# Optimization experiments

Measured on AMD Instinct MI355X. Metric: run time of the kernel, lower is better.

Reference implementation:

```python
import jax, jax.numpy as jnp
import numpy as np

D_MODEL = 768
D_AU = 5
D_VIS = 20
BOT = 64
WIN = 7
SCALE = 1.0 / np.sqrt(BOT).astype(np.float32)


def layernorm(x, w, b, eps=1e-5):
    mu = jnp.mean(x, axis=-1, keepdims=True)
    var = jnp.mean(jnp.square(x - mu), axis=-1, keepdims=True)
    return (x - mu) * jax.lax.rsqrt(var + eps) * w + b


def proximity_bias_matrix(prox_bias, L_a, L_v):
    # |i * (L_v/L_a) - j|, floored to int; gather into learned table, -inf outside window
    ai = jnp.arange(L_a, dtype=jnp.float32) * (L_v / L_a)  # [L_a]
    vj = jnp.arange(L_v, dtype=jnp.float32)                # [L_v]
    dist = jnp.floor(jnp.abs(ai[:, None] - vj[None, :])).astype(jnp.int32)  # [L_a, L_v]
    within = dist <= WIN
    gathered = prox_bias[jnp.clip(dist, 0, 2 * WIN)]
    return jnp.where(within, gathered, -jnp.inf)


def setup_inputs() -> dict:
    key = jax.random.key(0)
    ks = jax.random.split(key, 32)
    B, L_t, L_v, L_a = 32, 1024, 1024, 2048
    std = 0.02
    inp = {
        'x_text': jax.random.normal(ks[0], (B, L_t, D_MODEL), jnp.float32),
        'video_features': jax.random.normal(ks[1], (B, L_v, D_VIS), jnp.float32),
        'audio_features': jax.random.normal(ks[2], (B, L_a, D_AU), jnp.float32),
        # adapter input LayerNorm (BERT init: weight=1, bias=0)
        'ln_w': jnp.ones((D_MODEL,), jnp.float32),
        'ln_b': jnp.zeros((D_MODEL,), jnp.float32),
        # down projections (torch Linear: [out, in])
        'dpa_w': std * jax.random.normal(ks[3], (BOT, D_AU), jnp.float32),
        'dpa_b': jnp.zeros((BOT,), jnp.float32),
        'dpv_w': std * jax.random.normal(ks[4], (BOT, D_VIS), jnp.float32),
        'dpv_b': jnp.zeros((BOT,), jnp.float32),
        # audio->video cross attention
        'wq_a': std * jax.random.normal(ks[5], (BOT, BOT), jnp.float32),
        'wk_v': std * jax.random.normal(ks[6], (BOT, BOT), jnp.float32),
        'wv_v': std * jax.random.normal(ks[7], (BOT, BOT), jnp.float32),
        'prox_bias': jnp.zeros((2 * WIN + 1,), jnp.float32),
        # fusion MLP + LN
        'fln_w': jnp.ones((2 * BOT,), jnp.float32),
        'fln_b': jnp.zeros((2 * BOT,), jnp.float32),
        'w1f_w': std * jax.random.normal(ks[8], (BOT, 2 * BOT), jnp.float32),
        'w1f_b': jnp.zeros((BOT,), jnp.float32),
        'w2f_w': std * jax.random.normal(ks[9], (BOT, BOT), jnp.float32),
        'w2f_b': jnp.zeros((BOT,), jnp.float32),
        # text->sync alignment attention
        'wq_t': std * jax.random.normal(ks[10], (BOT, D_MODEL), jnp.float32),
        'wk_s': std * jax.random.normal(ks[11], (BOT, BOT), jnp.float32),
        'wv_s': std * jax.random.normal(ks[12], (BOT, BOT), jnp.float32),
        # up projection + learnable scalar
        'up_w': std * jax.random.normal(ks[13], (D_MODEL, BOT), jnp.float32),
        'up_b': jnp.zeros((D_MODEL,), jnp.float32),
        'scale': jnp.ones((1,), jnp.float32),
    }
    return inp


def reference(x_text, video_features, audio_features, ln_w, ln_b, dpa_w, dpa_b,
              dpv_w, dpv_b, wq_a, wk_v, wv_v, prox_bias, fln_w, fln_b,
              w1f_w, w1f_b, w2f_w, w2f_b, wq_t, wk_s, wv_s, up_w, up_b, scale):
    L_v = video_features.shape[1]
    L_a = audio_features.shape[1]
    # adapter_layernorm_option == 'in'
    xt = layernorm(x_text, ln_w, ln_b)
    # down projections + ReLU
    H_v = jax.nn.relu(jnp.einsum('bvf,df->bvd', video_features, dpv_w) + dpv_b)
    H_a = jax.nn.relu(jnp.einsum('baf,df->bad', audio_features, dpa_w) + dpa_b)
    # audio queries attend to video keys/values with proximity bias
    Q_a = jnp.einsum('bad,ed->bae', H_a, wq_a)
    K_v = jnp.einsum('bvd,ed->bve', H_v, wk_v)
    V_v = jnp.einsum('bvd,ed->bve', H_v, wv_v)
    scores = jnp.einsum('bad,bvd->bav', Q_a, K_v) * SCALE
    scores = scores + proximity_bias_matrix(prox_bias, L_a, L_v)[None]
    A = jax.nn.softmax(scores, axis=-1)  # dropout: eval-mode identity
    H_v_tilde = jnp.einsum('bav,bvd->bad', A, V_v)
    # fusion
    H_av = jnp.concatenate([H_a, H_v_tilde], axis=-1)  # [B, L_a, 2*BOT]
    H_av_n = layernorm(H_av, fln_w, fln_b)
    H_fused = jax.nn.relu(jnp.einsum('bac,dc->bad', H_av_n, w1f_w) + w1f_b)
    H_sync = jnp.einsum('bad,ed->bae', H_fused, w2f_w) + w2f_b
    # text -> sync alignment attention
    Q_t = jnp.einsum('btm,dm->btd', xt, wq_t)
    K_s = jnp.einsum('bad,ed->bae', H_sync, wk_s)
    V_s = jnp.einsum('bad,ed->bae', H_sync, wv_s)
    align = jax.nn.softmax(jnp.einsum('btd,bad->bta', Q_t, K_s) * SCALE, axis=-1)
    H_align = jnp.einsum('bta,bad->btd', align, V_s)
    up = jnp.einsum('btd,md->btm', H_align, up_w) + up_b
    return up * scale
```

## Files before the change

### kernel.cpp

```cpp
#include <hip/hip_runtime.h>

typedef unsigned short u16;
typedef unsigned int u32;

using frag8 = __attribute__((ext_vector_type(8))) short;
using facc4 = __attribute__((ext_vector_type(4))) float;

__device__ __forceinline__ float b2f(u16 u) {
  union { u32 i; float f; } v; v.i = ((u32)u) << 16; return v.f;
}
__device__ __forceinline__ u16 f2b(float f) {
  union { float f; u32 i; } v; v.f = f;
  u32 u = v.i;
  return (u16)((u + 0x7FFFu + ((u >> 16) & 1u)) >> 16);
}
__device__ __forceinline__ float ldin(const void* p, size_t i, bool bf) {
  return bf ? b2f(((const u16*)p)[i]) : ((const float*)p)[i];
}
__device__ __forceinline__ u16 ldb(const void* p, size_t i, bool bf) {
  return bf ? ((const u16*)p)[i] : f2b(((const float*)p)[i]);
}
__device__ __forceinline__ bool dt_bf16(const void* ones) {
  return *(const u32*)ones == 0x3F803F80u;
}
__device__ __forceinline__ void gload_lds16(const void* g, void* l) {
  __builtin_amdgcn_global_load_lds(
      (__attribute__((address_space(1))) void*)(g),
      (__attribute__((address_space(3))) void*)(l), 16, 0, 0);
}

#define LT 1024
#define LV 1024
#define LA 2048
#define DM 768

#define W_QA 0
#define W_KV 4096
#define W_VV 8192
#define W_1F 12288
#define W_2F 20480
#define W_KS 24576
#define W_VS 28672
#define W_UP 32768
#define W_QT 81920
#define W_TOT 131072

__global__ __launch_bounds__(256) void k_prep(
    const void* __restrict__ wqa, const void* __restrict__ wkv, const void* __restrict__ wvv,
    const void* __restrict__ w1f, const void* __restrict__ w2f,
    const void* __restrict__ wks, const void* __restrict__ wvs,
    const void* __restrict__ wup, const void* __restrict__ wqt, const void* __restrict__ lnw,
    u16* __restrict__ W)
{
  bool bf = dt_bf16(lnw);
  int idx = blockIdx.x * 256 + threadIdx.x;
  if (idx >= W_TOT) return;
  u16 v;
  if      (idx < W_KV) v = ldb(wqa, idx - W_QA, bf);
  else if (idx < W_VV) v = ldb(wkv, idx - W_KV, bf);
  else if (idx < W_1F) v = ldb(wvv, idx - W_VV, bf);
  else if (idx < W_2F) v = ldb(w1f, idx - W_1F, bf);
  else if (idx < W_KS) v = ldb(w2f, idx - W_2F, bf);
  else if (idx < W_VS) v = ldb(wks, idx - W_KS, bf);
  else if (idx < W_UP) v = ldb(wvs, idx - W_VS, bf);
  else if (idx < W_QT) v = ldb(wup, idx - W_UP, bf);
  else {
    int r = idx - W_QT;
    int k = r - (r / DM) * DM;
    v = f2b(ldin(wqt, r, bf) * ldin(lnw, k, bf));
  }
  W[idx] = v;
}

__global__ __launch_bounds__(256) void k_const(
    const u16* __restrict__ W, const void* __restrict__ wqt, const void* __restrict__ lnb,
    const void* __restrict__ dtp, float* __restrict__ CC)
{
  bool bf = dt_bf16(dtp);
  int j = blockIdx.x * 8 + (threadIdx.x >> 5);
  int lane32 = threadIdx.x & 31;
  float s = 0.f;
  if (j < 64) {
    for (int k = lane32; k < DM; k += 32) s += b2f(W[W_QT + (size_t)j * DM + k]);
  } else {
    int e = j - 64;
    for (int k = lane32; k < DM; k += 32)
      s += ldin(lnb, k, bf) * ldin(wqt, (size_t)e * DM + k, bf);
  }
#pragma unroll
  for (int m = 1; m < 32; m <<= 1) s += __shfl_xor(s, m);
  if (lane32 == 0) CC[j] = s;
}

__global__ __launch_bounds__(256) void k_video(
    const void* __restrict__ vid, const void* __restrict__ dpv_w, const void* __restrict__ dpv_b,
    const u16* __restrict__ W, const void* __restrict__ dtp,
    u16* __restrict__ KvG, u16* __restrict__ VvTG)
{
  bool bf = dt_bf16(dtp);
  __shared__ float vidT[20][72];
  __shared__ float dpvT[20][72];
  __shared__ float dpvB[64];
  __shared__ u16 hvL[64][72];
  __shared__ u16 ksS[64][72];
  __shared__ u16 vsS[64][72];
  int tid = threadIdx.x;
  int b = blockIdx.x >> 4, v0 = (blockIdx.x & 15) << 6;
  for (int c = tid; c < 1280; c += 256) {
    int row = c / 20, d = c - row * 20;
    vidT[d][row] = ldin(vid, (size_t)(b * LV + v0) * 20 + c, bf);
    dpvT[d][row] = ldin(dpv_w, c, bf);
  }
  if (tid < 64) dpvB[tid] = ldin(dpv_b, tid, bf);
  __syncthreads();
  int w = tid >> 6, ln = tid & 63;
  int quad = ln >> 4, l16 = ln & 15;
  for (int rr = 0; rr < 16; ++rr) {
    int row = w * 16 + rr;
    float h = dpvB[ln];
#pragma unroll
    for (int d = 0; d < 20; ++d) h += vidT[d][row] * dpvT[d][ln];
    hvL[row][ln] = f2b(fmaxf(h, 0.f));
  }
  facc4 ka[4] = {}, va[4] = {};
#pragma unroll
  for (int kk = 0; kk < 2; ++kk) {
    frag8 af = *(const frag8*)&hvL[w * 16 + l16][kk * 32 + quad * 8];
#pragma unroll
    for (int nt = 0; nt < 4; ++nt) {
      frag8 bk = *(const frag8*)(W + W_KV + (size_t)(nt * 16 + l16) * 64 + kk * 32 + quad * 8);
      frag8 bv = *(const frag8*)(W + W_VV + (size_t)(nt * 16 + l16) * 64 + kk * 32 + quad * 8);
      ka[nt] = __builtin_amdgcn_mfma_f32_16x16x32_bf16(af, bk, ka[nt], 0, 0, 0);
      va[nt] = __builtin_amdgcn_mfma_f32_16x16x32_bf16(af, bv, va[nt], 0, 0, 0);
    }
  }
#pragma unroll
  for (int nt = 0; nt < 4; ++nt)
#pragma unroll
    for (int r = 0; r < 4; ++r) {
      int row = w * 16 + quad * 4 + r;
      ksS[row][nt * 16 + l16] = f2b(ka[nt][r]);
      vsS[row][nt * 16 + l16] = f2b(va[nt][r]);
    }
  __syncthreads();
  for (int c = tid; c < 2048; c += 256) {
    int row = c >> 5, sg = c & 31;
    u32 v = (u32)ksS[row][sg * 2] | ((u32)ksS[row][sg * 2 + 1] << 16);
    *(u32*)(KvG + (size_t)(b * LV + v0 + row) * 64 + sg * 2) = v;
  }
  for (int c = tid; c < 2048; c += 256) {
    int e = c >> 5, sg = c & 31;
    u32 v = (u32)vsS[sg * 2][e] | ((u32)vsS[sg * 2 + 1][e] << 16);
    *(u32*)(VvTG + (size_t)(b * 64 + e) * LV + v0 + sg * 2) = v;
  }
}

__global__ __launch_bounds__(256, 4) void k_lnqt(
    const void* __restrict__ x, const u16* __restrict__ W, const float* __restrict__ CC,
    const void* __restrict__ dtp, u16* __restrict__ Qt)
{
  bool bf = dt_bf16(dtp);
  __shared__ __align__(16) char pool[40960];
  int tid = threadIdx.x;
  int w = tid >> 6, ln = tid & 63;
  int quad = ln >> 4, l16 = ln & 15;
  int rt = w >> 1;
  int nt0 = (w & 1) * 2;
  int R0 = blockIdx.x * 32;
  facc4 acc[2] = {};
  float s = 0.f, ss = 0.f;

  if (!bf) {
    int rq = ln >> 4;
    const char* xb = (const char*)x + (size_t)R0 * 3072;
    const char* p0 = xb + (size_t)(w * 8 + rq) * 3072 + (((ln & 15) ^ rq) << 4);
    const char* p1 = xb + (size_t)(w * 8 + 4 + rq) * 3072 + (((ln & 15) ^ (4 + rq)) << 4);
    const char* wgA = (const char*)(W + W_QT) +
        (size_t)(w * 16 + (ln >> 3)) * 1536 + (((ln & 7) ^ (ln >> 3)) << 4);
    const char* wgB = wgA + 8 * 1536;

#define STAGE_X(BUF, T) do { \
    size_t o_ = (size_t)(T) * 256; \
    char* lb_ = pool + (BUF) * 8192 + w * 2048; \
    gload_lds16(p0 + o_, lb_); \
    gload_lds16(p1 + o_, lb_ + 1024); \
  } while (0)

#define STAGE_W(BUF, T) do { \
    size_t o_ = (size_t)(T) * 128; \
    char* wb_ = pool + 24576 + (BUF) * 8192 + w * 2048; \
    gload_lds16(wgA + o_, wb_); \
    gload_lds16(wgB + o_, wb_ + 1024); \
  } while (0)

    int rbase = (rt * 16 + l16) * 256;
    int r8 = l16 & 7;
    int c0a = rbase + (((quad * 2) ^ r8) << 4);
    int c0b = rbase + (((quad * 2 + 1) ^ r8) << 4);
    int c1a = rbase + (((8 + quad * 2) ^ r8) << 4);
    int c1b = rbase + (((9 + quad * 2) ^ r8) << 4);
    int wo0 = l16 * 128 + ((quad ^ r8) << 4);
    int wo1 = l16 * 128 + (((4 + quad) ^ r8) << 4);

#define COMPUTE(XB, WB) do { \
    const char* xt_ = pool + (XB) * 8192; \
    const char* wt_ = pool + 24576 + (WB) * 8192; \
    _Pragma("unroll") \
    for (int ks = 0; ks < 2; ++ks) { \
      float4 v0 = *(const float4*)(xt_ + (ks ? c1a : c0a)); \
      float4 v1 = *(const float4*)(xt_ + (ks ? c1b : c0b)); \
      s += v0.x + v0.y + v0.z + v0.w + v1.x + v1.y + v1.z + v1.w; \
      ss += v0.x * v0.x + v0.y * v0.y + v0.z * v0.z + v0.w * v0.w \
          + v1.x * v1.x + v1.y * v1.y + v1.z * v1.z + v1.w * v1.w; \
      union { u16 a[8]; frag8 f; } af; \
      af.a[0] = f2b(v0.x); af.a[1] = f2b(v0.y); af.a[2] = f2b(v0.z); af.a[3] = f2b(v0.w); \
      af.a[4] = f2b(v1.x); af.a[5] = f2b(v1.y); af.a[6] = f2b(v1.z); af.a[7] = f2b(v1.w); \
      int wo_ = ks ? wo1 : wo0; \
      _Pragma("unroll") \
      for (int n = 0; n < 2; ++n) { \
        frag8 bfr = *(const frag8*)(wt_ + wo_ + (nt0 + n) * 2048); \
        acc[n] = __builtin_amdgcn_mfma_f32_16x16x32_bf16(af.f, bfr, acc[n], 0, 0, 0); \
      } \
    } \
  } while (0)

#define ITERA(T, XC, XN, WN) do { \
    asm volatile("s_waitcnt vmcnt(2)" ::: "memory"); \
    __builtin_amdgcn_s_barrier(); \
    STAGE_W(WN, (T) + 1); \
    STAGE_X(XN, (T) + 2); \
    COMPUTE(XC, (T) & 1); \
  } while (0)

    STAGE_W(0, 0);
    STAGE_X(0, 0);
    STAGE_X(1, 1);
    ITERA(0, 0, 2, 1);
    ITERA(1, 1, 0, 0);
    ITERA(2, 2, 1, 1);
    ITERA(3, 0, 2, 0);
    ITERA(4, 1, 0, 1);
    ITERA(5, 2, 1, 0);
    ITERA(6, 0, 2, 1);
    ITERA(7, 1, 0, 0);
    ITERA(8, 2, 1, 1);
    ITERA(9, 0, 2, 0);
    asm volatile("s_waitcnt vmcnt(2)" ::: "memory");
    __builtin_amdgcn_s_barrier();
    STAGE_W(1, 11);
    COMPUTE(1, 0);
    asm volatile("s_waitcnt vmcnt(0)" ::: "memory");
    __builtin_amdgcn_s_barrier();
    COMPUTE(2, 1);

#undef ITERA
#undef COMPUTE
#undef STAGE_W
#undef STAGE_X
  } else {
    const u16* xrowb = (const u16*)x + (size_t)(R0 + rt * 16 + l16) * DM + quad * 8;
    for (int c = 0; c < 24; ++c) {
      union { u16 a[8]; frag8 f; } af;
      af.f = *(const frag8*)(xrowb + c * 32);
#pragma unroll
      for (int jj = 0; jj < 8; ++jj) { float v = b2f(af.a[jj]); s += v; ss += v * v; }
      int col = c * 32 + quad * 8;
#pragma unroll
      for (int n = 0; n < 2; ++n) {
        frag8 bfr = *(const frag8*)(W + W_QT + (size_t)((nt0 + n) * 16 + l16) * DM + col);
        acc[n] = __builtin_amdgcn_mfma_f32_16x16x32_bf16(af.f, bfr, acc[n], 0, 0, 0);
      }
    }
  }

  s += __shfl_xor(s, 16); ss += __shfl_xor(ss, 16);
  s += __shfl_xor(s, 32); ss += __shfl_xor(ss, 32);
  float mu = s * (1.f / 768.f);
  float var = ss * (1.f / 768.f) - mu * mu;
  float rs = rsqrtf(var + 1e-5f);
  float muR[4], rsR[4];
#pragma unroll
  for (int r = 0; r < 4; ++r) {
    muR[r] = __shfl(mu, quad * 4 + r);
    rsR[r] = __shfl(rs, quad * 4 + r);
  }
#pragma unroll
  for (int n = 0; n < 2; ++n) {
    int ntg = nt0 + n;
    float c1 = CC[ntg * 16 + l16], c2 = CC[64 + ntg * 16 + l16];
#pragma unroll
    for (int r = 0; r < 4; ++r) {
      int lrow = rt * 16 + quad * 4 + r;
      Qt[(size_t)(R0 + lrow) * 64 + ntg * 16 + l16] =
          f2b((acc[n][r] - muR[r] * c1) * rsR[r] * 0.125f + c2 * 0.125f);
    }
  }
}

__global__ __launch_bounds__(256, 4) void k_audio(
    const void* __restrict__ audio, const void* __restrict__ dpa_w, const void* __restrict__ dpa_b,
    const void* __restrict__ prox_b,
    const void* __restrict__ fln_w, const void* __restrict__ fln_b,
    const void* __restrict__ w1f_b, const void* __restrict__ w2f_b,
    const u16* __restrict__ W, const void* __restrict__ dtp,
    const u16* __restrict__ KvG, const u16* __restrict__ VvTG,
    u16* __restrict__ KsG, u16* __restrict__ VsTG)
{
  bool bf = dt_bf16(dtp);
  __shared__ __align__(16) char pool[36928];
  u16* S0   = (u16*)pool;
  u16* qL   = (u16*)(pool + 9216);
  u16* hnL  = (u16*)(pool + 18432);
  u16* vsS  = (u16*)(pool + 9216);
  float* flnw = (float*)(pool + 35840);
  float* flnb = (float*)(pool + 36352);
  float* prox = (float*)(pool + 36864);

  int tid = threadIdx.x;
  int b = blockIdx.x >> 5, i0 = (blockIdx.x & 31) << 6;
  int w = tid >> 6, ln = tid & 63;
  int quad = ln >> 4, l16 = ln & 15;
  int jbase = (i0 >> 1) - 8;

  if (tid >= 64 && tid < 192) { int t = tid - 64; flnw[t] = ldin(fln_w, t, bf); flnb[t] = ldin(fln_b, t, bf); }
  if (tid >= 192 && tid < 207) prox[tid - 192] = ldin(prox_b, tid - 192, bf);
  __syncthreads();

  float haF[4][4];
  {
    frag8 au = {};
    if (quad == 0) {
      size_t base = (size_t)(b * LA + i0 + w * 16 + l16) * 5;
#pragma unroll
      for (int k = 0; k < 5; ++k) au[k] = (short)ldb(audio, base + k, bf);
    }
#pragma unroll
    for (int nt = 0; nt < 4; ++nt) {
      frag8 bd = {};
      if (quad == 0) {
#pragma unroll
        for (int k = 0; k < 5; ++k) bd[k] = (short)ldb(dpa_w, (size_t)(nt * 16 + l16) * 5 + k, bf);
      }
      facc4 z = {};
      facc4 ha = __builtin_amdgcn_mfma_f32_16x16x32_bf16(au, bd, z, 0, 0, 0);
      float dB = ldin(dpa_b, nt * 16 + l16, bf);
#pragma unroll
      for (int r = 0; r < 4; ++r) {
        u16 hb = f2b(fmaxf(ha[r] + dB, 0.f));
        S0[(w * 16 + quad * 4 + r) * 72 + nt * 16 + l16] = hb;
        haF[nt][r] = b2f(hb);
      }
    }
  }
  {
    facc4 qa[4] = {};
#pragma unroll
    for (int kk = 0; kk < 2; ++kk) {
      frag8 af = *(const frag8*)&S0[(w * 16 + l16) * 72 + kk * 32 + quad * 8];
#pragma unroll
      for (int nt = 0; nt < 4; ++nt) {
        frag8 bfr = *(const frag8*)(W + W_QA + (size_t)(nt * 16 + l16) * 64 + kk * 32 + quad * 8);
        qa[nt] = __builtin_amdgcn_mfma_f32_16x16x32_bf16(af, bfr, qa[nt], 0, 0, 0);
      }
    }
#pragma unroll
    for (int nt = 0; nt < 4; ++nt)
#pragma unroll
      for (int r = 0; r < 4; ++r)
        qL[(w * 16 + quad * 4 + r) * 72 + nt * 16 + l16] = f2b(qa[nt][r] * 0.125f);
  }
  float inv[4];
  {
    facc4 sa[3] = {};
#pragma unroll
    for (int kk = 0; kk < 2; ++kk) {
      frag8 af = *(const frag8*)&qL[(w * 16 + l16) * 72 + kk * 32 + quad * 8];
#pragma unroll
      for (int nt = 0; nt < 3; ++nt) {
        int jj = jbase + nt * 16 + l16;
        jj = jj < 0 ? 0 : (jj > LV - 1 ? LV - 1 : jj);
        frag8 bfr = *(const frag8*)(KvG + ((size_t)(b * LV + jj) << 6) + kk * 32 + quad * 8);
        sa[nt] = __builtin_amdgcn_mfma_f32_16x16x32_bf16(af, bfr, sa[nt], 0, 0, 0);
      }
    }
    float den[4] = {0.f, 0.f, 0.f, 0.f};
#pragma unroll
    for (int nt = 0; nt < 3; ++nt)
#pragma unroll
      for (int r = 0; r < 4; ++r) {
        int row16 = quad * 4 + r;
        int i = i0 + w * 16 + row16;
        int j = jbase + nt * 16 + l16;
        float dist = fabsf((float)i * 0.5f - (float)j);
        float p = 0.f;
        if (j >= 0 && j < LV && dist < 8.f)
          p = exp2f(fminf(sa[nt][r] + prox[(int)dist], 60.f) * 1.44269504f);
        u16 pb = f2b(p);
        den[r] += b2f(pb);
        S0[(w * 16 + row16) * 72 + nt * 16 + l16] = pb;
      }
#pragma unroll
    for (int r = 0; r < 4; ++r) {
      S0[(w * 16 + quad * 4 + r) * 72 + 48 + l16] = 0;
#pragma unroll
      for (int m = 1; m < 16; m <<= 1) den[r] += __shfl_xor(den[r], m);
      inv[r] = 1.f / den[r];
    }
  }
  float hvF[4][4];
  {
    facc4 ha[4] = {};
#pragma unroll
    for (int kk = 0; kk < 2; ++kk) {
      frag8 af = *(const frag8*)&S0[(w * 16 + l16) * 72 + kk * 32 + quad * 8];
#pragma unroll
      for (int nt = 0; nt < 4; ++nt) {
        const u16* vp = VvTG + (size_t)(b * 64 + nt * 16 + l16) * LV;
        frag8 bfr = *(const frag8*)(vp + jbase + kk * 32 + quad * 8);
        ha[nt] = __builtin_amdgcn_mfma_f32_16x16x32_bf16(af, bfr, ha[nt], 0, 0, 0);
      }
    }
#pragma unroll
    for (int nt = 0; nt < 4; ++nt)
#pragma unroll
      for (int r = 0; r < 4; ++r) {
        u16 hb = f2b(ha[nt][r] * inv[r]);
        hvF[nt][r] = b2f(hb);
      }
  }
  __syncthreads();
#pragma unroll
  for (int r = 0; r < 4; ++r) {
    float s = 0.f, ss = 0.f;
#pragma unroll
    for (int nt = 0; nt < 4; ++nt) {
      float a = haF[nt][r], c = hvF[nt][r];
      s += a + c; ss += a * a + c * c;
    }
#pragma unroll
    for (int m = 1; m < 16; m <<= 1) { s += __shfl_xor(s, m); ss += __shfl_xor(ss, m); }
    float mu = s * (1.f / 128.f);
    float var = ss * (1.f / 128.f) - mu * mu;
    float rs = rsqrtf(var + 1e-5f);
    int row = w * 16 + quad * 4 + r;
#pragma unroll
    for (int nt = 0; nt < 4; ++nt) {
      int col = nt * 16 + l16;
      hnL[row * 136 + col]      = f2b((haF[nt][r] - mu) * rs * flnw[col] + flnb[col]);
      hnL[row * 136 + 64 + col] = f2b((hvF[nt][r] - mu) * rs * flnw[64 + col] + flnb[64 + col]);
    }
  }
  {
    facc4 f1[4] = {};
#pragma unroll
    for (int kk = 0; kk < 4; ++kk) {
      frag8 af = *(const frag8*)&hnL[(w * 16 + l16) * 136 + kk * 32 + quad * 8];
#pragma unroll
      for (int nt = 0; nt < 4; ++nt) {
        frag8 bfr = *(const frag8*)(W + W_1F + (size_t)(nt * 16 + l16) * 128 + kk * 32 + quad * 8);
        f1[nt] = __builtin_amdgcn_mfma_f32_16x16x32_bf16(af, bfr, f1[nt], 0, 0, 0);
      }
    }
#pragma unroll
    for (int nt = 0; nt < 4; ++nt) {
      float b1 = ldin(w1f_b, nt * 16 + l16, bf);
#pragma unroll
      for (int r = 0; r < 4; ++r)
        S0[(w * 16 + quad * 4 + r) * 72 + nt * 16 + l16] = f2b(fmaxf(f1[nt][r] + b1, 0.f));
    }
  }
  {
    facc4 f2[4] = {};
#pragma unroll
    for (int kk = 0; kk < 2; ++kk) {
      frag8 af = *(const frag8*)&S0[(w * 16 + l16) * 72 + kk * 32 + quad * 8];
#pragma unroll
      for (int nt = 0; nt < 4; ++nt) {
        frag8 bfr = *(const frag8*)(W + W_2F + (size_t)(nt * 16 + l16) * 64 + kk * 32 + quad * 8);
        f2[nt] = __builtin_amdgcn_mfma_f32_16x16x32_bf16(af, bfr, f2[nt], 0, 0, 0);
      }
    }
#pragma unroll
    for (int nt = 0; nt < 4; ++nt) {
      float b2 = ldin(w2f_b, nt * 16 + l16, bf);
#pragma unroll
      for (int r = 0; r < 4; ++r)
        S0[(w * 16 + quad * 4 + r) * 72 + nt * 16 + l16] = f2b(f2[nt][r] + b2);
    }
  }
  {
    facc4 fk[4] = {}, fv[4] = {};
#pragma unroll
    for (int kk = 0; kk < 2; ++kk) {
      frag8 af = *(const frag8*)&S0[(w * 16 + l16) * 72 + kk * 32 + quad * 8];
#pragma unroll
      for (int nt = 0; nt < 4; ++nt) {
        frag8 bk = *(const frag8*)(W + W_KS + (size_t)(nt * 16 + l16) * 64 + kk * 32 + quad * 8);
        frag8 bv = *(const frag8*)(W + W_VS + (size_t)(nt * 16 + l16) * 64 + kk * 32 + quad * 8);
        fk[nt] = __builtin_amdgcn_mfma_f32_16x16x32_bf16(af, bk, fk[nt], 0, 0, 0);
        fv[nt] = __builtin_amdgcn_mfma_f32_16x16x32_bf16(af, bv, fv[nt], 0, 0, 0);
      }
    }
#pragma unroll
    for (int nt = 0; nt < 4; ++nt)
#pragma unroll
      for (int r = 0; r < 4; ++r) {
        int row = w * 16 + quad * 4 + r;
        S0[row * 72 + nt * 16 + l16]  = f2b(fk[nt][r]);
        vsS[row * 72 + nt * 16 + l16] = f2b(fv[nt][r]);
      }
  }
  __syncthreads();
  for (int c = tid; c < 2048; c += 256) {
    int row = c >> 5, sg = c & 31;
    u32 v = (u32)S0[row * 72 + sg * 2] | ((u32)S0[row * 72 + sg * 2 + 1] << 16);
    *(u32*)(KsG + (size_t)(b * LA + i0 + row) * 64 + sg * 2) = v;
  }
  for (int c = tid; c < 2048; c += 256) {
    int e = c >> 5, sg = c & 31;
    u32 v = (u32)vsS[sg * 2 * 72 + e] | ((u32)vsS[(sg * 2 + 1) * 72 + e] << 16);
    *(u32*)(VsTG + (size_t)(b * 64 + e) * LA + i0 + sg * 2) = v;
  }
}

#define KS_OFF 0
#define VT_OFF 16384
#define PO_OFF 32768

__global__ __launch_bounds__(256, 4) void k_attn_p(
    const u16* __restrict__ Qt, const u16* __restrict__ KsG, const u16* __restrict__ VsT,
    u16* __restrict__ OpG, float* __restrict__ DenG)
{
  __shared__ __align__(16) char pool[40960];
  int tid = threadIdx.x, w = tid >> 6, ln = tid & 63;
  int quad = ln >> 4, l16 = ln & 15;
  int pb = blockIdx.x;
  int b = pb >> 5, tt = (pb >> 1) & 15, half = pb & 1;
  int t0 = tt << 6;
  const u16* qp = Qt + (size_t)(b * LT + t0 + w * 16 + l16) * 64;
  frag8 qf0 = *(const frag8*)(qp + quad * 8);
  frag8 qf1 = *(const frag8*)(qp + 32 + quad * 8);

  int r8 = ln >> 3;
  int sgx = (ln & 7) ^ r8;
  const char* kg0 = (const char*)KsG +
      (((size_t)(b * LA + half * 1024 + w * 16 + r8)) << 7) + sgx * 16;
  const char* kg1 = kg0 + 1024;
  const char* vg0 = (const char*)VsT +
      (((size_t)(b * 64 + w * 16 + r8)) * LA + half * 1024 + sgx * 8) * 2;
  const char* vg1 = vg0 + (size_t)8 * LA * 2;

#define STAGE(BUF, TT) do { \
    size_t ko_ = (size_t)(TT) * 8192, vo_ = (size_t)(TT) * 128; \
    gload_lds16(kg0 + ko_, pool + KS_OFF + (BUF) * 8192 + w * 2048); \
    gload_lds16(kg1 + ko_, pool + KS_OFF + (BUF) * 8192 + w * 2048 + 1024); \
    gload_lds16(vg0 + vo_, pool + VT_OFF + (BUF) * 8192 + w * 2048); \
    gload_lds16(vg1 + vo_, pool + VT_OFF + (BUF) * 8192 + w * 2048 + 1024); \
  } while (0)

  int l8 = l16 & 7, lh = l16 >> 3;
  int swl = l8 << 4;
  int koff0 = l16 * 128 + ((quad * 16) ^ swl);
  int koff1 = l16 * 128 + ((64 + quad * 16) ^ swl);
  int pro0 = w * 2048 + l16 * 128 + ((quad ^ l8) << 4);
  int pro1 = w * 2048 + l16 * 128 + (((4 + quad) ^ l8) << 4);
  int pwb = w * 2048 + quad * 512 + l8 * 2;

  facc4 oacc[4] = {};
  float den[4] = {0.f, 0.f, 0.f, 0.f};

#define COMPUTE(CUR) do { \
    const char* ksp_ = pool + KS_OFF + (CUR) * 8192; \
    const char* vtp_ = pool + VT_OFF + (CUR) * 8192; \
    __builtin_amdgcn_s_setprio(1); \
    _Pragma("unroll") \
    for (int nt = 0; nt < 4; ++nt) { \
      frag8 b0 = *(const frag8*)(ksp_ + koff0 + nt * 2048); \
      frag8 b1 = *(const frag8*)(ksp_ + koff1 + nt * 2048); \
      facc4 sv = {}; \
      sv = __builtin_amdgcn_mfma_f32_16x16x32_bf16(qf0, b0, sv, 0, 0, 0); \
      sv = __builtin_amdgcn_mfma_f32_16x16x32_bf16(qf1, b1, sv, 0, 0, 0); \
      _Pragma("unroll") \
      for (int r = 0; r < 4; ++r) { \
        float p = exp2f(fminf(sv[r], 60.f) * 1.44269504f); \
        u16 pb_ = f2b(p); \
        den[r] += b2f(pb_); \
        int rm_ = ((quad & 1) << 2) + r; \
        *(u16*)(pool + PO_OFF + pwb + r * 128 + (((nt * 2 + lh) ^ rm_) << 4)) = pb_; \
      } \
    } \
    _Pragma("unroll") \
    for (int kk = 0; kk < 2; ++kk) { \
      frag8 af = *(const frag8*)(pool + PO_OFF + (kk ? pro1 : pro0)); \
      _Pragma("unroll") \
      for (int nt = 0; nt < 4; ++nt) { \
        frag8 bv = *(const frag8*)(vtp_ + (kk ? koff1 : koff0) + nt * 2048); \
        oacc[nt] = __builtin_amdgcn_mfma_f32_16x16x32_bf16(af, bv, oacc[nt], 0, 0, 0); \
      } \
    } \
    __builtin_amdgcn_s_setprio(0); \
  } while (0)

#define ITERS(TT, CUR) do { \
    asm volatile("s_waitcnt vmcnt(0)" ::: "memory"); \
    __builtin_amdgcn_s_barrier(); \
    STAGE((CUR) ^ 1, (TT) + 1); \
    COMPUTE(CUR); \
  } while (0)

  STAGE(0, 0);
  for (int t2 = 0; t2 < 14; t2 += 2) {
    ITERS(t2, 0);
    ITERS(t2 + 1, 1);
  }
  ITERS(14, 0);
  asm volatile("s_waitcnt vmcnt(0)" ::: "memory");
  __builtin_amdgcn_s_barrier();
  COMPUTE(1);

#undef ITERS
#undef COMPUTE
#undef STAGE

#pragma unroll
  for (int m = 1; m < 16; m <<= 1)
#pragma unroll
    for (int r = 0; r < 4; ++r) den[r] += __shfl_xor(den[r], m);
  if (l16 == 0) {
#pragma unroll
    for (int r = 0; r < 4; ++r)
      DenG[(size_t)pb * 64 + w * 16 + quad * 4 + r] = den[r];
  }
#pragma unroll
  for (int nt = 0; nt < 4; ++nt)
#pragma unroll
    for (int r = 0; r < 4; ++r)
      OpG[(size_t)pb * 4096 + (w * 16 + quad * 4 + r) * 64 + nt * 16 + l16] =
          f2b(oacc[nt][r]);
}

__global__ __launch_bounds__(256) void k_up(
    const u16* __restrict__ OpG, const float* __restrict__ DenG,
    const u16* __restrict__ W, const void* __restrict__ up_b,
    const void* __restrict__ scaleP, const void* __restrict__ dtp, void* __restrict__ outp)
{
  bool bf = dt_bf16(dtp);
  int tid = threadIdx.x, w = tid >> 6, ln = tid & 63;
  int quad = ln >> 4, l16 = ln & 15;
  int g = blockIdx.x;
  int b = g >> 5, tt = (g >> 1) & 15, nh = g & 1;
  int t0 = tt << 6;
  int blk = b * 16 + tt;
  int row = w * 16 + l16;
  const u16* p0 = OpG + ((size_t)blk * 2 + 0) * 4096 + row * 64;
  const u16* p1 = p0 + 4096;
  float dsum = DenG[(size_t)blk * 128 + row] + DenG[(size_t)blk * 128 + 64 + row];
  float inv = 1.f / dsum;
  union { u16 a[8]; frag8 f; } a0, a1;
  {
    frag8 u0 = *(const frag8*)(p0 + quad * 8);
    frag8 u1 = *(const frag8*)(p1 + quad * 8);
    frag8 v0 = *(const frag8*)(p0 + 32 + quad * 8);
    frag8 v1 = *(const frag8*)(p1 + 32 + quad * 8);
#pragma unroll
    for (int j = 0; j < 8; ++j) {
      a0.a[j] = f2b((b2f((u16)u0[j]) + b2f((u16)u1[j])) * inv);
      a1.a[j] = f2b((b2f((u16)v0[j]) + b2f((u16)v1[j])) * inv);
    }
  }
  float scl = ldin(scaleP, 0, bf);
  u16* o16 = (u16*)outp;
  float* o32 = (float*)outp;
  for (int nt = nh * 24; nt < nh * 24 + 24; ++nt) {
    frag8 b0f = *(const frag8*)(W + W_UP + (size_t)(nt * 16 + l16) * 64 + quad * 8);
    frag8 b1f = *(const frag8*)(W + W_UP + (size_t)(nt * 16 + l16) * 64 + 32 + quad * 8);
    facc4 d = {};
    d = __builtin_amdgcn_mfma_f32_16x16x32_bf16(a0.f, b0f, d, 0, 0, 0);
    d = __builtin_amdgcn_mfma_f32_16x16x32_bf16(a1.f, b1f, d, 0, 0, 0);
    float ub = ldin(up_b, nt * 16 + l16, bf);
#pragma unroll
    for (int r = 0; r < 4; ++r) {
      int t = t0 + w * 16 + quad * 4 + r;
      size_t idx = ((size_t)(b * LT) + t) * DM + nt * 16 + l16;
      float v = (d[r] + ub) * scl;
      if (bf) o16[idx] = f2b(v); else o32[idx] = v;
    }
  }
}

extern "C" void kernel_launch(void* const* d_in, const int* in_sizes, int n_in,
                              void* d_out, int out_size, void* d_ws, size_t ws_size,
                              hipStream_t stream) {
  const void* x_text = d_in[0];
  const void* video  = d_in[1];
  const void* audio  = d_in[2];
  const void* ln_w   = d_in[3];
  const void* ln_b   = d_in[4];
  const void* dpa_w  = d_in[5];
  const void* dpa_b  = d_in[6];
  const void* dpv_w  = d_in[7];
  const void* dpv_b  = d_in[8];
  const void* wq_a   = d_in[9];
  const void* wk_v   = d_in[10];
  const void* wv_v   = d_in[11];
  const void* prox   = d_in[12];
  const void* fln_w  = d_in[13];
  const void* fln_b  = d_in[14];
  const void* w1f_w  = d_in[15];
  const void* w1f_b  = d_in[16];
  const void* w2f_w  = d_in[17];
  const void* w2f_b  = d_in[18];
  const void* wq_t   = d_in[19];
  const void* wk_s   = d_in[20];
  const void* wv_s   = d_in[21];
  const void* up_w   = d_in[22];
  const void* up_b   = d_in[23];
  const void* scale  = d_in[24];

  char* ws = (char*)d_ws;
  u16* KvG  = (u16*)(ws);
  u16* VvTG = (u16*)(ws + 4194304);
  u16* Qt   = (u16*)(ws + 8388608);
  u16* KsG  = (u16*)(ws + 12582912);
  u16* VsTG = (u16*)(ws + 20971520);
  u16* W    = (u16*)(ws + 29360128);
  float* CC = (float*)(ws + 29622272);
  u16* OpG  = (u16*)(ws);
  float* DenG = (float*)(ws + 29622784);

  k_prep <<<dim3(512), dim3(256), 0, stream>>>(wq_a, wk_v, wv_v, w1f_w, w2f_w,
                                               wk_s, wv_s, up_w, wq_t, ln_w, W);
  k_const<<<dim3(16),  dim3(256), 0, stream>>>(W, wq_t, ln_b, ln_w, CC);
  k_video<<<dim3(512), dim3(256), 0, stream>>>(video, dpv_w, dpv_b, W, ln_w, KvG, VvTG);
  k_lnqt <<<dim3(1024), dim3(256), 0, stream>>>(x_text, W, CC, ln_w, Qt);
  k_audio<<<dim3(1024), dim3(256), 0, stream>>>(audio, dpa_w, dpa_b, prox,
                                                fln_w, fln_b, w1f_b, w2f_b,
                                                W, ln_w, KvG, VvTG, KsG, VsTG);
  k_attn_p<<<dim3(1024), dim3(256), 0, stream>>>(Qt, KsG, VsTG, OpG, DenG);
  k_up   <<<dim3(1024), dim3(256), 0, stream>>>(OpG, DenG, W, up_b, scale, ln_w, d_out);
}
```

Measured before the change: 364.9 us.

## Merge independent prep, const, video, lnqt and audio kernels into two launches

Folds weight prep, the LN constant computation and the video projection into one launch by splitting on block index, and merges the text LN+Q projection with the audio branch into a second launch. This removes launch gaps and lets independent stages share the GPU concurrently. To break dependencies inside a launch, the constant and video parts now read raw weights directly instead of the prepped bf16 buffer, adding some redundant conversion work and scalar loads. The merged k_mid block carries the larger LDS pool of the two paths, which may lower occupancy for the audio blocks.

After: 394.8 us. 1.08x slower.

```diff
diff --git a/kernel.cpp b/kernel.cpp
--- a/kernel.cpp
+++ b/kernel.cpp
@@ -45,67 +45,67 @@
 #define W_QT 81920
 #define W_TOT 131072
 
-__global__ __launch_bounds__(256) void k_prep(
+__global__ __launch_bounds__(256) void k_stage0(
     const void* __restrict__ wqa, const void* __restrict__ wkv, const void* __restrict__ wvv,
     const void* __restrict__ w1f, const void* __restrict__ w2f,
     const void* __restrict__ wks, const void* __restrict__ wvs,
-    const void* __restrict__ wup, const void* __restrict__ wqt, const void* __restrict__ lnw,
-    u16* __restrict__ W)
+    const void* __restrict__ wup, const void* __restrict__ wqt,
+    const void* __restrict__ lnw, const void* __restrict__ lnb,
+    const void* __restrict__ vid, const void* __restrict__ dpv_w, const void* __restrict__ dpv_b,
+    u16* __restrict__ W, float* __restrict__ CC,
+    u16* __restrict__ KvG, u16* __restrict__ VvTG)
 {
   bool bf = dt_bf16(lnw);
-  int idx = blockIdx.x * 256 + threadIdx.x;
-  if (idx >= W_TOT) return;
-  u16 v;
-  if      (idx < W_KV) v = ldb(wqa, idx - W_QA, bf);
-  else if (idx < W_VV) v = ldb(wkv, idx - W_KV, bf);
-  else if (idx < W_1F) v = ldb(wvv, idx - W_VV, bf);
-  else if (idx < W_2F) v = ldb(w1f, idx - W_1F, bf);
-  else if (idx < W_KS) v = ldb(w2f, idx - W_2F, bf);
-  else if (idx < W_VS) v = ldb(wks, idx - W_KS, bf);
-  else if (idx < W_UP) v = ldb(wvs, idx - W_VS, bf);
-  else if (idx < W_QT) v = ldb(wup, idx - W_UP, bf);
-  else {
-    int r = idx - W_QT;
-    int k = r - (r / DM) * DM;
-    v = f2b(ldin(wqt, r, bf) * ldin(lnw, k, bf));
-  }
-  W[idx] = v;
-}
-
-__global__ __launch_bounds__(256) void k_const(
-    const u16* __restrict__ W, const void* __restrict__ wqt, const void* __restrict__ lnb,
-    const void* __restrict__ dtp, float* __restrict__ CC)
-{
-  bool bf = dt_bf16(dtp);
-  int j = blockIdx.x * 8 + (threadIdx.x >> 5);
-  int lane32 = threadIdx.x & 31;
-  float s = 0.f;
-  if (j < 64) {
-    for (int k = lane32; k < DM; k += 32) s += b2f(W[W_QT + (size_t)j * DM + k]);
-  } else {
-    int e = j - 64;
-    for (int k = lane32; k < DM; k += 32)
-      s += ldin(lnb, k, bf) * ldin(wqt, (size_t)e * DM + k, bf);
-  }
-#pragma unroll
-  for (int m = 1; m < 32; m <<= 1) s += __shfl_xor(s, m);
-  if (lane32 == 0) CC[j] = s;
-}
-
-__global__ __launch_bounds__(256) void k_video(
-    const void* __restrict__ vid, const void* __restrict__ dpv_w, const void* __restrict__ dpv_b,
-    const u16* __restrict__ W, const void* __restrict__ dtp,
-    u16* __restrict__ KvG, u16* __restrict__ VvTG)
-{
-  bool bf = dt_bf16(dtp);
+  int bid = blockIdx.x;
+  int tid = threadIdx.x;
+
+  if (bid < 512) {
+    int idx = bid * 256 + tid;
+    if (idx >= W_TOT) return;
+    u16 v;
+    if      (idx < W_KV) v = ldb(wqa, idx - W_QA, bf);
+    else if (idx < W_VV) v = ldb(wkv, idx - W_KV, bf);
+    else if (idx < W_1F) v = ldb(wvv, idx - W_VV, bf);
+    else if (idx < W_2F) v = ldb(w1f, idx - W_1F, bf);
+    else if (idx < W_KS) v = ldb(w2f, idx - W_2F, bf);
+    else if (idx < W_VS) v = ldb(wks, idx - W_KS, bf);
+    else if (idx < W_UP) v = ldb(wvs, idx - W_VS, bf);
+    else if (idx < W_QT) v = ldb(wup, idx - W_UP, bf);
+    else {
+      int r = idx - W_QT;
+      int k = r - (r / DM) * DM;
+      v = f2b(ldin(wqt, r, bf) * ldin(lnw, k, bf));
+    }
+    W[idx] = v;
+    return;
+  }
+
+  if (bid < 528) {
+    int j = (bid - 512) * 8 + (tid >> 5);
+    int lane32 = tid & 31;
+    float s = 0.f;
+    if (j < 64) {
+      for (int k = lane32; k < DM; k += 32)
+        s += b2f(f2b(ldin(wqt, (size_t)j * DM + k, bf) * ldin(lnw, k, bf)));
+    } else {
+      int e = j - 64;
+      for (int k = lane32; k < DM; k += 32)
+        s += ldin(lnb, k, bf) * ldin(wqt, (size_t)e * DM + k, bf);
+    }
+#pragma unroll
+    for (int m = 1; m < 32; m <<= 1) s += __shfl_xor(s, m);
+    if (lane32 == 0) CC[j] = s;
+    return;
+  }
+
   __shared__ float vidT[20][72];
   __shared__ float dpvT[20][72];
   __shared__ float dpvB[64];
   __shared__ u16 hvL[64][72];
   __shared__ u16 ksS[64][72];
   __shared__ u16 vsS[64][72];
-  int tid = threadIdx.x;
-  int b = blockIdx.x >> 4, v0 = (blockIdx.x & 15) << 6;
+  int vb = bid - 528;
+  int b = vb >> 4, v0 = (vb & 15) << 6;
   for (int c = tid; c < 1280; c += 256) {
     int row = c / 20, d = c - row * 20;
     vidT[d][row] = ldin(vid, (size_t)(b * LV + v0) * 20 + c, bf);
@@ -128,10 +128,15 @@
     frag8 af = *(const frag8*)&hvL[w * 16 + l16][kk * 32 + quad * 8];
 #pragma unroll
     for (int nt = 0; nt < 4; ++nt) {
-      frag8 bk = *(const frag8*)(W + W_KV + (size_t)(nt * 16 + l16) * 64 + kk * 32 + quad * 8);
-      frag8 bv = *(const frag8*)(W + W_VV + (size_t)(nt * 16 + l16) * 64 + kk * 32 + quad * 8);
-      ka[nt] = __builtin_amdgcn_mfma_f32_16x16x32_bf16(af, bk, ka[nt], 0, 0, 0);
-      va[nt] = __builtin_amdgcn_mfma_f32_16x16x32_bf16(af, bv, va[nt], 0, 0, 0);
+      union { u16 a[8]; frag8 f; } tk, tv;
+      size_t base = (size_t)(nt * 16 + l16) * 64 + kk * 32 + quad * 8;
+#pragma unroll
+      for (int j = 0; j < 8; ++j) {
+        tk.a[j] = ldb(wkv, base + j, bf);
+        tv.a[j] = ldb(wvv, base + j, bf);
+      }
+      ka[nt] = __builtin_amdgcn_mfma_f32_16x16x32_bf16(af, tk.f, ka[nt], 0, 0, 0);
+      va[nt] = __builtin_amdgcn_mfma_f32_16x16x32_bf16(af, tv.f, va[nt], 0, 0, 0);
     }
   }
 #pragma unroll
@@ -155,29 +160,38 @@
   }
 }
 
-__global__ __launch_bounds__(256, 4) void k_lnqt(
+__global__ __launch_bounds__(256, 4) void k_mid(
     const void* __restrict__ x, const u16* __restrict__ W, const float* __restrict__ CC,
-    const void* __restrict__ dtp, u16* __restrict__ Qt)
+    u16* __restrict__ Qt,
+    const void* __restrict__ audio, const void* __restrict__ dpa_w, const void* __restrict__ dpa_b,
+    const void* __restrict__ prox_b,
+    const void* __restrict__ fln_w, const void* __restrict__ fln_b,
+    const void* __restrict__ w1f_b, const void* __restrict__ w2f_b,
+    const u16* __restrict__ KvG, const u16* __restrict__ VvTG,
+    u16* __restrict__ KsG, u16* __restrict__ VsTG,
+    const void* __restrict__ dtp)
 {
   bool bf = dt_bf16(dtp);
   __shared__ __align__(16) char pool[40960];
   int tid = threadIdx.x;
   int w = tid >> 6, ln = tid & 63;
   int quad = ln >> 4, l16 = ln & 15;
-  int rt = w >> 1;
-  int nt0 = (w & 1) * 2;
-  int R0 = blockIdx.x * 32;
-  facc4 acc[2] = {};
-  float s = 0.f, ss = 0.f;
-
-  if (!bf) {
-    int rq = ln >> 4;
-    const char* xb = (const char*)x + (size_t)R0 * 3072;
-    const char* p0 = xb + (size_t)(w * 8 + rq) * 3072 + (((ln & 15) ^ rq) << 4);
-    const char* p1 = xb + (size_t)(w * 8 + 4 + rq) * 3072 + (((ln & 15) ^ (4 + rq)) << 4);
-    const char* wgA = (const char*)(W + W_QT) +
-        (size_t)(w * 16 + (ln >> 3)) * 1536 + (((ln & 7) ^ (ln >> 3)) << 4);
-    const char* wgB = wgA + 8 * 1536;
+
+  if (blockIdx.x < 1024) {
+    int rt = w >> 1;
+    int nt0 = (w & 1) * 2;
+    int R0 = blockIdx.x * 32;
+    facc4 acc[2] = {};
+    float s = 0.f, ss = 0.f;
+
+    if (!bf) {
+      int rq = ln >> 4;
+      const char* xb = (const char*)x + (size_t)R0 * 3072;
+      const char* p0 = xb + (size_t)(w * 8 + rq) * 3072 + (((ln & 15) ^ rq) << 4);
+      const char* p1 = xb + (size_t)(w * 8 + 4 + rq) * 3072 + (((ln & 15) ^ (4 + rq)) << 4);
+      const char* wgA = (const char*)(W + W_QT) +
+          (size_t)(w * 16 + (ln >> 3)) * 1536 + (((ln & 7) ^ (ln >> 3)) << 4);
+      const char* wgB = wgA + 8 * 1536;
 
 #define STAGE_X(BUF, T) do { \
     size_t o_ = (size_t)(T) * 256; \
@@ -193,14 +207,14 @@
     gload_lds16(wgB + o_, wb_ + 1024); \
   } while (0)
 
-    int rbase = (rt * 16 + l16) * 256;
-    int r8 = l16 & 7;
-    int c0a = rbase + (((quad * 2) ^ r8) << 4);
-    int c0b = rbase + (((quad * 2 + 1) ^ r8) << 4);
-    int c1a = rbase + (((8 + quad * 2) ^ r8) << 4);
-    int c1b = rbase + (((9 + quad * 2) ^ r8) << 4);
-    int wo0 = l16 * 128 + ((quad ^ r8) << 4);
-    int wo1 = l16 * 128 + (((4 + quad) ^ r8) << 4);
+      int rbase = (rt * 16 + l16) * 256;
+      int r8 = l16 & 7;
+      int c0a = rbase + (((quad * 2) ^ r8) << 4);
+      int c0b = rbase + (((quad * 2 + 1) ^ r8) << 4);
+      int c1a = rbase + (((8 + quad * 2) ^ r8) << 4);
+      int c1b = rbase + (((9 + quad * 2) ^ r8) << 4);
+      int wo0 = l16 * 128 + ((quad ^ r8) << 4);
+      int wo1 = l16 * 128 + (((4 + quad) ^ r8) << 4);
 
 #define COMPUTE(XB, WB) do { \
     const char* xt_ = pool + (XB) * 8192; \
@@ -232,82 +246,72 @@
     COMPUTE(XC, (T) & 1); \
   } while (0)
 
-    STAGE_W(0, 0);
-    STAGE_X(0, 0);
-    STAGE_X(1, 1);
-    ITERA(0, 0, 2, 1);
-    ITERA(1, 1, 0, 0);
-    ITERA(2, 2, 1, 1);
-    ITERA(3, 0, 2, 0);
-    ITERA(4, 1, 0, 1);
-    ITERA(5, 2, 1, 0);
-    ITERA(6, 0, 2, 1);
-    ITERA(7, 1, 0, 0);
-    ITERA(8, 2, 1, 1);
-    ITERA(9, 0, 2, 0);
-    asm volatile("s_waitcnt vmcnt(2)" ::: "memory");
-    __builtin_amdgcn_s_barrier();
-    STAGE_W(1, 11);
-    COMPUTE(1, 0);
-    asm volatile("s_waitcnt vmcnt(0)" ::: "memory");
-    __builtin_amdgcn_s_barrier();
-    COMPUTE(2, 1);
+      STAGE_W(0, 0);
+      STAGE_X(0, 0);
+      STAGE_X(1, 1);
+      ITERA(0, 0, 2, 1);
+      ITERA(1, 1, 0, 0);
+      ITERA(2, 2, 1, 1);
+      ITERA(3, 0, 2, 0);
+      ITERA(4, 1, 0, 1);
+      ITERA(5, 2, 1, 0);
+      ITERA(6, 0, 2, 1);
+      ITERA(7, 1, 0, 0);
+      ITERA(8, 2, 1, 1);
+      ITERA(9, 0, 2, 0);
+      asm volatile("s_waitcnt vmcnt(2)" ::: "memory");
+      __builtin_amdgcn_s_barrier();
+      STAGE_W(1, 11);
+      COMPUTE(1, 0);
+      asm volatile("s_waitcnt vmcnt(0)" ::: "memory");
+      __builtin_amdgcn_s_barrier();
+      COMPUTE(2, 1);
 
 #undef ITERA
 #undef COMPUTE
 #undef STAGE_W
 #undef STAGE_X
-  } else {
-    const u16* xrowb = (const u16*)x + (size_t)(R0 + rt * 16 + l16) * DM + quad * 8;
-    for (int c = 0; c < 24; ++c) {
-      union { u16 a[8]; frag8 f; } af;
-      af.f = *(const frag8*)(xrowb + c * 32);
-#pragma unroll
-      for (int jj = 0; jj < 8; ++jj) { float v = b2f(af.a[jj]); s += v; ss += v * v; }
-      int col = c * 32 + quad * 8;
-#pragma unroll
-      for (int n = 0; n < 2; ++n) {
-        frag8 bfr = *(const frag8*)(W + W_QT + (size_t)((nt0 + n) * 16 + l16) * DM + col);
-        acc[n] = __builtin_amdgcn_mfma_f32_16x16x32_bf16(af.f, bfr, acc[n], 0, 0, 0);
-      }
-    }
-  }
-
-  s += __shfl_xor(s, 16); ss += __shfl_xor(ss, 16);
-  s += __shfl_xor(s, 32); ss += __shfl_xor(ss, 32);
-  float mu = s * (1.f / 768.f);
-  float var = ss * (1.f / 768.f) - mu * mu;
-  float rs = rsqrtf(var + 1e-5f);
-  float muR[4], rsR[4];
-#pragma unroll
-  for (int r = 0; r < 4; ++r) {
-    muR[r] = __shfl(mu, quad * 4 + r);
-    rsR[r] = __shfl(rs, quad * 4 + r);
-  }
-#pragma unroll
-  for (int n = 0; n < 2; ++n) {
-    int ntg = nt0 + n;
-    float c1 = CC[ntg * 16 + l16], c2 = CC[64 + ntg * 16 + l16];
+    } else {
+      const u16* xrowb = (const u16*)x + (size_t)(R0 + rt * 16 + l16) * DM + quad * 8;
+      for (int c = 0; c < 24; ++c) {
+        union { u16 a[8]; frag8 f; } af;
+        af.f = *(const frag8*)(xrowb + c * 32);
+#pragma unroll
+        for (int jj = 0; jj < 8; ++jj) { float v = b2f(af.a[jj]); s += v; ss += v * v; }
+        int col = c * 32 + quad * 8;
+#pragma unroll
+        for (int n = 0; n < 2; ++n) {
+          frag8 bfr = *(const frag8*)(W + W_QT + (size_t)((nt0 + n) * 16 + l16) * DM + col);
+          acc[n] = __builtin_amdgcn_mfma_f32_16x16x32_bf16(af.f, bfr, acc[n], 0, 0, 0);
+        }
+      }
+    }
+
+    s += __shfl_xor(s, 16); ss += __shfl_xor(ss, 16);
+    s += __shfl_xor(s, 32); ss += __shfl_xor(ss, 32);
+    float mu = s * (1.f / 768.f);
+    float var = ss * (1.f / 768.f) - mu * mu;
+    float rs = rsqrtf(var + 1e-5f);
+    float muR[4], rsR[4];
 #pragma unroll
     for (int r = 0; r < 4; ++r) {
-      int lrow = rt * 16 + quad * 4 + r;
-      Qt[(size_t)(R0 + lrow) * 64 + ntg * 16 + l16] =
-          f2b((acc[n][r] - muR[r] * c1) * rsR[r] * 0.125f + c2 * 0.125f);
-    }
-  }
-}
-
-__global__ __launch_bounds__(256, 4) void k_audio(
-    const void* __restrict__ audio, const void* __restrict__ dpa_w, const void* __restrict__ dpa_b,
-    const void* __restrict__ prox_b,
-    const void* __restrict__ fln_w, const void* __restrict__ fln_b,
-    const void* __restrict__ w1f_b, const void* __restrict__ w2f_b,
-    const u16* __restrict__ W, const void* __restrict__ dtp,
-    const u16* __restrict__ KvG, const u16* __restrict__ VvTG,
-    u16* __restrict__ KsG, u16* __restrict__ VsTG)
-{
-  bool bf = dt_bf16(dtp);
-  __shared__ __align__(16) char pool[36928];
+      muR[r] = __shfl(mu, quad * 4 + r);
+      rsR[r] = __shfl(rs, quad * 4 + r);
+    }
+#pragma unroll
+    for (int n = 0; n < 2; ++n) {
+      int ntg = nt0 + n;
+      float c1 = CC[ntg * 16 + l16], c2 = CC[64 + ntg * 16 + l16];
+#pragma unroll
+      for (int r = 0; r < 4; ++r) {
+        int lrow = rt * 16 + quad * 4 + r;
+        Qt[(size_t)(R0 + lrow) * 64 + ntg * 16 + l16] =
+            f2b((acc[n][r] - muR[r] * c1) * rsR[r] * 0.125f + c2 * 0.125f);
+      }
+    }
+    return;
+  }
+
   u16* S0   = (u16*)pool;
   u16* qL   = (u16*)(pool + 9216);
   u16* hnL  = (u16*)(pool + 18432);
@@ -316,10 +320,8 @@
   float* flnb = (float*)(pool + 36352);
   float* prox = (float*)(pool + 36864);
 
-  int tid = threadIdx.x;
-  int b = blockIdx.x >> 5, i0 = (blockIdx.x & 31) << 6;
-  int w = tid >> 6, ln = tid & 63;
-  int quad = ln >> 4, l16 = ln & 15;
+  int abid = blockIdx.x - 1024;
+  int b = abid >> 5, i0 = (abid & 31) << 6;
   int jbase = (i0 >> 1) - 8;
 
   if (tid >= 64 && tid < 192) { int t = tid - 64; flnw[t] = ldin(fln_w, t, bf); flnb[t] = ldin(fln_b, t, bf); }
@@ -728,14 +730,13 @@
   u16* OpG  = (u16*)(ws);
   float* DenG = (float*)(ws + 29622784);
 
-  k_prep <<<dim3(512), dim3(256), 0, stream>>>(wq_a, wk_v, wv_v, w1f_w, w2f_w,
-                                               wk_s, wv_s, up_w, wq_t, ln_w, W);
-  k_const<<<dim3(16),  dim3(256), 0, stream>>>(W, wq_t, ln_b, ln_w, CC);
-  k_video<<<dim3(512), dim3(256), 0, stream>>>(video, dpv_w, dpv_b, W, ln_w, KvG, VvTG);
-  k_lnqt <<<dim3(1024), dim3(256), 0, stream>>>(x_text, W, CC, ln_w, Qt);
-  k_audio<<<dim3(1024), dim3(256), 0, stream>>>(audio, dpa_w, dpa_b, prox,
-                                                fln_w, fln_b, w1f_b, w2f_b,
-                                                W, ln_w, KvG, VvTG, KsG, VsTG);
+  k_stage0<<<dim3(1040), dim3(256), 0, stream>>>(
+      wq_a, wk_v, wv_v, w1f_w, w2f_w, wk_s, wv_s, up_w, wq_t, ln_w, ln_b,
+      video, dpv_w, dpv_b, W, CC, KvG, VvTG);
+  k_mid<<<dim3(2048), dim3(256), 0, stream>>>(
+      x_text, W, CC, Qt,
+      audio, dpa_w, dpa_b, prox, fln_w, fln_b, w1f_b, w2f_b,
+      KvG, VvTG, KsG, VsTG, ln_w);
   k_attn_p<<<dim3(1024), dim3(256), 0, stream>>>(Qt, KsG, VsTG, OpG, DenG);
   k_up   <<<dim3(1024), dim3(256), 0, stream>>>(OpG, DenG, W, up_b, scale, ln_w, d_out);
 }
```
